# Performance work log

Measured on AMD Instinct MI355X. Metric: run time of the kernel, lower is better.

Reference implementation:

```python
import jax, jax.numpy as jnp
import numpy as np

D = 512       # d_model
H = 8         # n_heads
HD = D // H   # head_dim
LYR = 4       # number_of_layers
PMT = 20      # pmt_len
L = 2048      # decode / target length (src_len - pmt_len)
BS = 1
DOUT = 3      # d_output (3 coding classes)
DFF = 4 * D
EPS = 1e-5


def layer_norm(x, g, b):
    m = jnp.mean(x, axis=-1, keepdims=True)
    v = jnp.mean((x - m) ** 2, axis=-1, keepdims=True)
    return (x - m) * jax.lax.rsqrt(v + EPS) * g + b


def rope(x):
    # x: (b, h, s, hd); half-split rotary with base 10000, positions = arange(s)
    half = x.shape[-1] // 2
    pos = jnp.arange(x.shape[2], dtype=jnp.float32)
    inv_freq = 1.0 / (10000.0 ** (jnp.arange(half, dtype=jnp.float32) / half))
    ang = pos[:, None] * inv_freq[None, :]          # (s, half)
    cos = jnp.cos(ang)[None, None]                  # (1,1,s,half)
    sin = jnp.sin(ang)[None, None]
    x1, x2 = x[..., :half], x[..., half:]
    return jnp.concatenate([x1 * cos - x2 * sin, x1 * sin + x2 * cos], axis=-1)


def mha(xq, xkv, wqkv, bqkv, wo, bo, key_mask, causal):
    # xq: (b, sq, D), xkv: (b, sk, D); key_mask: (b, sk) with 1=valid
    b, sq, _ = xq.shape
    sk = xkv.shape[1]
    q = xq @ wqkv[:, :D] + bqkv[:D]
    kv = xkv @ wqkv[:, D:] + bqkv[D:]
    k, v = kv[..., :D], kv[..., D:]
    q = q.reshape(b, sq, H, HD).transpose(0, 2, 1, 3)   # (b,h,sq,hd)
    k = k.reshape(b, sk, H, HD).transpose(0, 2, 1, 3)
    v = v.reshape(b, sk, H, HD).transpose(0, 2, 1, 3)
    q = rope(q)
    k = rope(k)
    scores = jnp.einsum('bhqd,bhkd->bhqk', q, k) / jnp.sqrt(jnp.float32(HD))
    scores = scores + jnp.where(key_mask[:, None, None, :] > 0, 0.0, -1e9)
    if causal:
        cm = jnp.tril(jnp.ones((sq, sk), dtype=bool))
        scores = jnp.where(cm[None, None], scores, -1e9)
    attn = jax.nn.softmax(scores, axis=-1)
    out = jnp.einsum('bhqk,bhkd->bhqd', attn, v)
    out = out.transpose(0, 2, 1, 3).reshape(b, sq, D)
    return out @ wo + bo


def setup_inputs() -> dict:
    key = jax.random.key(0)
    ks = jax.random.split(key, 16)
    s = 0.02
    p = lambda i, shape: jax.random.normal(ks[i], shape, jnp.float32) * s
    return {
        'trg_inputs': jax.random.normal(ks[0], (BS, L, DOUT), jnp.float32),
        'src_rep': jax.random.normal(ks[1], (BS, PMT + L, D), jnp.float32),
        'src_mask': jnp.ones((BS, L), jnp.float32),
        'emb_w': p(2, (DOUT, D)), 'emb_b': jnp.zeros((D,), jnp.float32),
        'sa_wqkv': p(3, (LYR, D, 3 * D)), 'sa_bqkv': jnp.zeros((LYR, 3 * D), jnp.float32),
        'sa_wo': p(4, (LYR, D, D)), 'sa_bo': jnp.zeros((LYR, D), jnp.float32),
        'ca_wqkv': p(5, (LYR, D, 3 * D)), 'ca_bqkv': jnp.zeros((LYR, 3 * D), jnp.float32),
        'ca_wo': p(6, (LYR, D, D)), 'ca_bo': jnp.zeros((LYR, D), jnp.float32),
        'ffn_w1': p(7, (LYR, D, DFF)), 'ffn_b1': jnp.zeros((LYR, DFF), jnp.float32),
        'ffn_w2': p(8, (LYR, DFF, D)), 'ffn_b2': jnp.zeros((LYR, D), jnp.float32),
        'ln_g': jnp.ones((LYR, 3, D), jnp.float32), 'ln_b': jnp.zeros((LYR, 3, D), jnp.float32),
        'lnf_g': jnp.ones((D,), jnp.float32), 'lnf_b': jnp.zeros((D,), jnp.float32),
        'gen_w': p(9, (D, DOUT)), 'gen_b': jnp.zeros((DOUT,), jnp.float32),
    }


def reference(trg_inputs, src_rep, src_mask, emb_w, emb_b, sa_wqkv, sa_bqkv, sa_wo, sa_bo,
              ca_wqkv, ca_bqkv, ca_wo, ca_bo, ffn_w1, ffn_b1, ffn_w2, ffn_b2,
              ln_g, ln_b, lnf_g, lnf_b, gen_w, gen_b):
    srb = src_rep[:, PMT:, :]                       # (bs, L, D)
    x = trg_inputs @ emb_w + emb_b                  # (bs, L, D)
    trg_mask = src_mask                             # parallel mode: trg_mask = src_mask
    for li in range(LYR):
        h = layer_norm(x, ln_g[li, 0], ln_b[li, 0])
        x = x + mha(h, h, sa_wqkv[li], sa_bqkv[li], sa_wo[li], sa_bo[li], trg_mask, causal=True)
        h = layer_norm(x, ln_g[li, 1], ln_b[li, 1])
        x = x + mha(h, srb, ca_wqkv[li], ca_bqkv[li], ca_wo[li], ca_bo[li], src_mask, causal=False)
        h = layer_norm(x, ln_g[li, 2], ln_b[li, 2])
        x = x + (jax.nn.relu(h @ ffn_w1[li] + ffn_b1[li]) @ ffn_w2[li] + ffn_b2[li])
    x = layer_norm(x, lnf_g, lnf_b)
    return x @ gen_w + gen_b                        # logits (bs, L, 3)
```

## Files before the change

kernel.cpp:

```cpp
#include <hip/hip_runtime.h>
#include <hip/hip_bf16.h>

#define SEQ 2048
#define DM 512
#define NHEAD 8
#define HDIM 64
#define DFFN 2048
#define PMTN 20

typedef __bf16 bf16x8 __attribute__((ext_vector_type(8)));
typedef float f32x4 __attribute__((ext_vector_type(4)));
typedef unsigned short u16x8 __attribute__((ext_vector_type(8)));

__device__ __forceinline__ float wave_sum(float v) {
#pragma unroll
  for (int off = 32; off; off >>= 1) v += __shfl_xor(v, off);
  return v;
}

__device__ __forceinline__ unsigned short f2b(float x) {
  __hip_bfloat16 h = __float2bfloat16(x);
  return *(unsigned short*)&h;
}

__device__ __forceinline__ void gll16(const __hip_bfloat16* g, __hip_bfloat16* l) {
  __builtin_amdgcn_global_load_lds(
      (const __attribute__((address_space(1))) unsigned int*)(g),
      (__attribute__((address_space(3))) unsigned int*)(l), 16, 0, 0);
}

__global__ __launch_bounds__(256) void embed_kernel(
    const float* __restrict__ trg, const float* __restrict__ w,
    const float* __restrict__ b, float* __restrict__ X) {
  int idx = blockIdx.x * 256 + threadIdx.x;
  int r = idx >> 9, c = idx & 511;
  float t0 = trg[r * 3 + 0], t1 = trg[r * 3 + 1], t2 = trg[r * 3 + 2];
  X[idx] = t0 * w[c] + t1 * w[512 + c] + t2 * w[1024 + c] + b[c];
}

__global__ __launch_bounds__(256) void cast_bf16_kernel(
    const float* __restrict__ in, __hip_bfloat16* __restrict__ out) {
  int i = blockIdx.x * 256 + threadIdx.x;
  out[i] = __float2bfloat16(in[i]);
}

__global__ __launch_bounds__(256) void rope_table_kernel(float2* __restrict__ rt) {
  int idx = blockIdx.x * 256 + threadIdx.x;
  int row = idx >> 5, i = idx & 31;
  float inv = __expf(-(float)i * (9.210340371976184f / 32.f));
  float sn, cs;
  sincosf((float)row * inv, &sn, &cs);
  rt[idx] = make_float2(cs, sn);
}

__global__ __launch_bounds__(256) void mbias_kernel(
    const float* __restrict__ mask, float* __restrict__ mb) {
  int i = blockIdx.x * 256 + threadIdx.x;
  mb[i] = (mask[i] > 0.f) ? 0.f : -8.0e9f;
}

__global__ __launch_bounds__(256) void ln_bf16_kernel(
    const float* __restrict__ x, const float* __restrict__ g,
    const float* __restrict__ b, __hip_bfloat16* __restrict__ o) {
  int row = blockIdx.x * 4 + (threadIdx.x >> 6);
  int lane = threadIdx.x & 63;
  const float* xr = x + (long)row * DM;
  float v[8];
  float s = 0.f;
#pragma unroll
  for (int j = 0; j < 8; j++) { v[j] = xr[lane + 64 * j]; s += v[j]; }
  s = wave_sum(s);
  float mean = s * (1.f / DM);
  float q = 0.f;
#pragma unroll
  for (int j = 0; j < 8; j++) { float d = v[j] - mean; q += d * d; }
  q = wave_sum(q);
  float r = rsqrtf(q * (1.f / DM) + 1e-5f);
  __hip_bfloat16* orow = o + (long)row * DM;
#pragma unroll
  for (int j = 0; j < 8; j++) {
    int c = lane + 64 * j;
    orow[c] = __float2bfloat16((v[j] - mean) * r * g[c] + b[c]);
  }
}

__global__ __launch_bounds__(256) void ln_f32_kernel(
    const float* __restrict__ x, const float* __restrict__ g,
    const float* __restrict__ b, float* __restrict__ o) {
  int row = blockIdx.x * 4 + (threadIdx.x >> 6);
  int lane = threadIdx.x & 63;
  const float* xr = x + (long)row * DM;
  float v[8];
  float s = 0.f;
#pragma unroll
  for (int j = 0; j < 8; j++) { v[j] = xr[lane + 64 * j]; s += v[j]; }
  s = wave_sum(s);
  float mean = s * (1.f / DM);
  float q = 0.f;
#pragma unroll
  for (int j = 0; j < 8; j++) { float d = v[j] - mean; q += d * d; }
  q = wave_sum(q);
  float r = rsqrtf(q * (1.f / DM) + 1e-5f);
  float* orow = o + (long)row * DM;
#pragma unroll
  for (int j = 0; j < 8; j++) {
    int c = lane + 64 * j;
    orow[c] = (v[j] - mean) * r * g[c] + b[c];
  }
}

__global__ __launch_bounds__(256) void transpose_layer_kernel(
    const float* __restrict__ wqkv, const float* __restrict__ wo,
    const float* __restrict__ cwqkv, const float* __restrict__ cwo,
    const float* __restrict__ w1, const float* __restrict__ w2,
    __hip_bfloat16* __restrict__ Wt) {
  int b = blockIdx.x;
  const float* W;
  __hip_bfloat16* O;
  int Kd, Nd;
  if (b < 192)      { W = wqkv;  O = Wt + 0;       Kd = 512;  Nd = 1536; }
  else if (b < 256) { W = wo;    O = Wt + 786432;  Kd = 512;  Nd = 512;  b -= 192; }
  else if (b < 448) { W = cwqkv; O = Wt + 1048576; Kd = 512;  Nd = 1536; b -= 256; }
  else if (b < 512) { W = cwo;   O = Wt + 1835008; Kd = 512;  Nd = 512;  b -= 448; }
  else if (b < 768) { W = w1;    O = Wt + 2097152; Kd = 512;  Nd = 2048; b -= 512; }
  else              { W = w2;    O = Wt + 3145728; Kd = 2048; Nd = 512;  b -= 768; }
  int tn = Nd >> 6;
  int k0 = (b / tn) * 64, n0 = (b % tn) * 64;
  __shared__ float T[64][65];
  int t = threadIdx.x;
  int rr = t >> 4, c4 = (t & 15) * 4;
#pragma unroll
  for (int p = 0; p < 4; p++) {
    int row = rr + p * 16;
    float4 v = *(const float4*)(W + (long)(k0 + row) * Nd + n0 + c4);
    T[row][c4 + 0] = v.x; T[row][c4 + 1] = v.y;
    T[row][c4 + 2] = v.z; T[row][c4 + 3] = v.w;
  }
  __syncthreads();
#pragma unroll
  for (int p = 0; p < 4; p++) {
    int row = rr + p * 16;
    ushort4 pk;
    pk.x = f2b(T[c4 + 0][row]); pk.y = f2b(T[c4 + 1][row]);
    pk.z = f2b(T[c4 + 2][row]); pk.w = f2b(T[c4 + 3][row]);
    *(ushort4*)(O + (long)(n0 + row) * Kd + k0 + c4) = pk;
  }
}

__global__ __launch_bounds__(256) void gemm_bf16_64(
    const __hip_bfloat16* __restrict__ A, int lda,
    const __hip_bfloat16* __restrict__ Bt, int ldb,
    const float* __restrict__ bias,
    const float* __restrict__ residual,
    float* __restrict__ Cf, __hip_bfloat16* __restrict__ Cb,
    int ldc, int K, int relu) {
  __shared__ __attribute__((aligned(16))) __hip_bfloat16 As[2][4096];
  __shared__ __attribute__((aligned(16))) __hip_bfloat16 Bs[2][4096];
  const int t = threadIdx.x;
  const int n0 = blockIdx.x * 64, m0 = blockIdx.y * 64;
  const int w = t >> 6, lane = t & 63;
  const int wr = w >> 1, wc = w & 1;
  const int fr = lane & 15, fk = lane >> 4;
  const int r0 = t & 63, c0 = t >> 6;
  const __hip_bfloat16* Arow = A + (long)(m0 + r0) * lda;
  const __hip_bfloat16* Brow = Bt + (long)(n0 + r0) * ldb;

  uint4 ra0 = *(const uint4*)(Arow + c0 * 8);
  uint4 ra1 = *(const uint4*)(Arow + (c0 + 4) * 8);
  uint4 rb0 = *(const uint4*)(Brow + c0 * 8);
  uint4 rb1 = *(const uint4*)(Brow + (c0 + 4) * 8);
  *(uint4*)(&As[0][(c0 * 64 + r0) * 8]) = ra0;
  *(uint4*)(&As[0][((c0 + 4) * 64 + r0) * 8]) = ra1;
  *(uint4*)(&Bs[0][(c0 * 64 + r0) * 8]) = rb0;
  *(uint4*)(&Bs[0][((c0 + 4) * 64 + r0) * 8]) = rb1;
  __syncthreads();

  f32x4 acc[2][2] = {};
  const int NK = K >> 6;
  for (int ks = 0; ks < NK; ++ks) {
    const int cur = ks & 1;
    if (ks + 1 < NK) {
      const int ko = (ks + 1) << 6;
      ra0 = *(const uint4*)(Arow + ko + c0 * 8);
      ra1 = *(const uint4*)(Arow + ko + (c0 + 4) * 8);
      rb0 = *(const uint4*)(Brow + ko + c0 * 8);
      rb1 = *(const uint4*)(Brow + ko + (c0 + 4) * 8);
    }
#pragma unroll
    for (int kk = 0; kk < 2; ++kk) {
      const int kc = kk * 4 + fk;
      bf16x8 a0 = *(const bf16x8*)(&As[cur][(kc * 64 + wr * 32 + fr) * 8]);
      bf16x8 a1 = *(const bf16x8*)(&As[cur][(kc * 64 + wr * 32 + 16 + fr) * 8]);
      bf16x8 b0 = *(const bf16x8*)(&Bs[cur][(kc * 64 + wc * 32 + fr) * 8]);
      bf16x8 b1 = *(const bf16x8*)(&Bs[cur][(kc * 64 + wc * 32 + 16 + fr) * 8]);
      acc[0][0] = __builtin_amdgcn_mfma_f32_16x16x32_bf16(a0, b0, acc[0][0], 0, 0, 0);
      acc[0][1] = __builtin_amdgcn_mfma_f32_16x16x32_bf16(a0, b1, acc[0][1], 0, 0, 0);
      acc[1][0] = __builtin_amdgcn_mfma_f32_16x16x32_bf16(a1, b0, acc[1][0], 0, 0, 0);
      acc[1][1] = __builtin_amdgcn_mfma_f32_16x16x32_bf16(a1, b1, acc[1][1], 0, 0, 0);
    }
    if (ks + 1 < NK) {
      const int nxt = cur ^ 1;
      *(uint4*)(&As[nxt][(c0 * 64 + r0) * 8]) = ra0;
      *(uint4*)(&As[nxt][((c0 + 4) * 64 + r0) * 8]) = ra1;
      *(uint4*)(&Bs[nxt][(c0 * 64 + r0) * 8]) = rb0;
      *(uint4*)(&Bs[nxt][((c0 + 4) * 64 + r0) * 8]) = rb1;
    }
    __syncthreads();
  }

#pragma unroll
  for (int m = 0; m < 2; ++m)
#pragma unroll
    for (int n = 0; n < 2; ++n)
#pragma unroll
      for (int j = 0; j < 4; ++j) {
        int r = m0 + wr * 32 + m * 16 + fk * 4 + j;
        int c = n0 + wc * 32 + n * 16 + fr;
        float v = acc[m][n][j] + bias[c];
        if (relu) v = fmaxf(v, 0.f);
        if (residual) v += residual[(long)r * ldc + c];
        if (Cf) Cf[(long)r * ldc + c] = v;
        if (Cb) Cb[(long)r * ldc + c] = __float2bfloat16(v);
      }
}

__global__ __launch_bounds__(256) void pack_kernel(
    const __hip_bfloat16* __restrict__ qsrc, int ldq,
    const __hip_bfloat16* __restrict__ ksrc, int ldk,
    const __hip_bfloat16* __restrict__ vsrc, int ldv,
    const float2* __restrict__ rt,
    __hip_bfloat16* __restrict__ Qp, __hip_bfloat16* __restrict__ Kp,
    __hip_bfloat16* __restrict__ Vp) {
  const int row = blockIdx.x;
  const int t = threadIdx.x;
  const int h = t >> 5, i = t & 31;
  float2 cs = rt[row * 32 + i];
  const long dsto = ((long)h * SEQ + row) * 64 + i;
  {
    const __hip_bfloat16* p = qsrc + (long)row * ldq + h * 64;
    float a = __bfloat162float(p[i]), b = __bfloat162float(p[i + 32]);
    Qp[dsto] = __float2bfloat16(a * cs.x - b * cs.y);
    Qp[dsto + 32] = __float2bfloat16(a * cs.y + b * cs.x);
  }
  {
    const __hip_bfloat16* p = ksrc + (long)row * ldk + h * 64;
    float a = __bfloat162float(p[i]), b = __bfloat162float(p[i + 32]);
    Kp[dsto] = __float2bfloat16(a * cs.x - b * cs.y);
    Kp[dsto + 32] = __float2bfloat16(a * cs.y + b * cs.x);
  }
  {
    const __hip_bfloat16* p = vsrc + (long)row * ldv + h * 64;
    Vp[dsto] = p[i];
    Vp[dsto + 32] = p[i + 32];
  }
}

__global__ __launch_bounds__(256) void attn_part_kernel(
    const __hip_bfloat16* __restrict__ Qp, const __hip_bfloat16* __restrict__ Kp,
    const __hip_bfloat16* __restrict__ Vp, const float* __restrict__ mbias,
    __hip_bfloat16* __restrict__ Op, float* __restrict__ Ml,
    int causal, int csz) {
  const int qt = blockIdx.x, ch = blockIdx.y, head = blockIdx.z;
  const int kv0 = ch * csz;
  if (causal && kv0 > qt * 64 + 63) return;
  const int kvlen = causal ? min(csz, qt * 64 + 64 - kv0) : csz;
  const int nt = (kvlen + 63) >> 6;

  __shared__ __attribute__((aligned(16))) __hip_bfloat16 Ks[4096];
  __shared__ __attribute__((aligned(16))) __hip_bfloat16 Vt[4096];
  __shared__ __attribute__((aligned(16))) __hip_bfloat16 Ps[4096];
  const int t = threadIdx.x, w = t >> 6, lane = t & 63;
  const int fr = lane & 15, fk = lane >> 4;
  const int qr = qt * 64 + w * 16 + fr;
  const int wq0 = qt * 64 + w * 16;
  const float SCL = 0.18033688011112042f;

  bf16x8 qa0, qa1;
  {
    const __hip_bfloat16* qp = Qp + ((long)head * SEQ + qr) * 64 + fk * 8;
    qa0 = *(const bf16x8*)qp;
    qa1 = *(const bf16x8*)(qp + 32);
  }
  const __hip_bfloat16* Kh = Kp + (long)head * SEQ * 64;
  const __hip_bfloat16* Vh = Vp + (long)head * SEQ * 64;

  float m_i = -3e38f, l_i = 0.f;
  f32x4 o_[4] = {};
  const int sw2 = (fr & 7) << 4;

  const int skrow = t & 63, skc = t >> 6;
  const int vr = t & 31, vc = (t >> 5) & 7;

  for (int tile = 0; tile < nt; ++tile) {
    const int kb = kv0 + tile * 64;
    __syncthreads();
    {
      const __hip_bfloat16* src = Kh + (long)(kb + skrow) * 64 + skc * 8;
      gll16(src, Ks + t * 8);
      gll16(src + 32, Ks + t * 8 + 2048);
    }
    {
      const __hip_bfloat16* vp = Vh + (long)(kb + 2 * vr) * 64 + vc * 8;
      u16x8 v0 = *(const u16x8*)vp;
      u16x8 v1 = *(const u16x8*)(vp + 64);
#pragma unroll
      for (int e = 0; e < 8; e++) {
        int d = vc * 8 + e;
        ushort2 hh;
        hh.x = v0[e]; hh.y = v1[e];
        *(ushort2*)((char*)Vt + ((d * 128 + 4 * vr) ^ (e << 4))) = hh;
      }
    }
    __syncthreads();

    const bool need = !causal || (kb <= wq0 + 15);
    if (need) {
      const bool diag = causal && (kb + 63 > wq0);

      f32x4 sacc[4];
#pragma unroll
      for (int n = 0; n < 4; n++) {
        bf16x8 ka0 = *(const bf16x8*)(Ks + fk * 512 + (n * 16 + fr) * 8);
        bf16x8 ka1 = *(const bf16x8*)(Ks + (4 + fk) * 512 + (n * 16 + fr) * 8);
        f32x4 zz = {};
        zz = __builtin_amdgcn_mfma_f32_16x16x32_bf16(ka0, qa0, zz, 0, 0, 0);
        sacc[n] = __builtin_amdgcn_mfma_f32_16x16x32_bf16(ka1, qa1, zz, 0, 0, 0);
      }

      float sv[4][4];
      float rm = -3e38f;
#pragma unroll
      for (int n = 0; n < 4; n++) {
        const int ka = kb + n * 16 + fk * 4;
        float4 mb = *(const float4*)(mbias + ka);
        sv[n][0] = sacc[n][0] + mb.x;
        sv[n][1] = sacc[n][1] + mb.y;
        sv[n][2] = sacc[n][2] + mb.z;
        sv[n][3] = sacc[n][3] + mb.w;
        if (diag) {
#pragma unroll
          for (int j = 0; j < 4; j++)
            if (ka + j > qr) sv[n][j] = -3e38f;
        }
#pragma unroll
        for (int j = 0; j < 4; j++) rm = fmaxf(rm, sv[n][j]);
      }
      rm = fmaxf(rm, __shfl_xor(rm, 16));
      rm = fmaxf(rm, __shfl_xor(rm, 32));
      if (!__all(rm <= m_i)) {
        float nm = fmaxf(m_i, rm);
        float f = exp2f((m_i - nm) * SCL);
        l_i *= f;
#pragma unroll
        for (int n = 0; n < 4; n++) o_[n] *= f;
        m_i = nm;
      }
      float ps = 0.f;
#pragma unroll
      for (int n = 0; n < 4; n++) {
        float p0 = exp2f((sv[n][0] - m_i) * SCL);
        float p1 = exp2f((sv[n][1] - m_i) * SCL);
        float p2 = exp2f((sv[n][2] - m_i) * SCL);
        float p3 = exp2f((sv[n][3] - m_i) * SCL);
        ps += (p0 + p1) + (p2 + p3);
        ushort4 pk4;
        pk4.x = f2b(p0); pk4.y = f2b(p1); pk4.z = f2b(p2); pk4.w = f2b(p3);
        *(ushort4*)((char*)Ps + ((w * 2048 + fr * 128 + (n * 16 + fk * 4) * 2) ^ sw2)) = pk4;
      }
      ps += __shfl_xor(ps, 16);
      ps += __shfl_xor(ps, 32);
      l_i += ps;

#pragma unroll
      for (int s = 0; s < 2; s++) {
        bf16x8 pb = *(const bf16x8*)((char*)Ps + ((w * 2048 + fr * 128 + s * 64 + fk * 16) ^ sw2));
#pragma unroll
        for (int n = 0; n < 4; n++) {
          bf16x8 va = *(const bf16x8*)((char*)Vt + (((n * 16 + fr) * 128 + s * 64 + fk * 16) ^ sw2));
          o_[n] = __builtin_amdgcn_mfma_f32_16x16x32_bf16(va, pb, o_[n], 0, 0, 0);
        }
      }
    }
  }

  const long bid = ((long)head * 32 + qt) * gridDim.y + ch;
  __hip_bfloat16* Ob = Op + bid * 4096;
#pragma unroll
  for (int n = 0; n < 4; n++) {
    ushort4 ov;
    ov.x = f2b(o_[n][0]); ov.y = f2b(o_[n][1]);
    ov.z = f2b(o_[n][2]); ov.w = f2b(o_[n][3]);
    *(ushort4*)(Ob + (w * 16 + fr) * 64 + n * 16 + fk * 4) = ov;
  }
  if (fk == 0) {
    float2 ml = make_float2(m_i, l_i);
    *(float2*)(Ml + bid * 128 + (w * 16 + fr) * 2) = ml;
  }
}

__global__ __launch_bounds__(256) void attn_combine_kernel(
    const __hip_bfloat16* __restrict__ Op, const float* __restrict__ Ml,
    __hip_bfloat16* __restrict__ O, int ldo, int causal, int csz, int nch) {
  const int qt = blockIdx.x, head = blockIdx.y;
  const int nc = causal ? min(nch, (qt * 64 + 63) / csz + 1) : nch;
  const int t = threadIdx.x;
  const int row = t >> 2, c16 = (t & 3) * 16;
  const long bid0 = ((long)head * 32 + qt) * nch;
  const float SCL = 0.18033688011112042f;
  float M = -3e38f;
  for (int c = 0; c < nc; c++) M = fmaxf(M, Ml[(bid0 + c) * 128 + row * 2]);
  float L = 0.f;
  float acc[16] = {};
  for (int c = 0; c < nc; c++) {
    float2 ml = *(const float2*)(Ml + (bid0 + c) * 128 + row * 2);
    float wg = exp2f((ml.x - M) * SCL);
    L += wg * ml.y;
    const __hip_bfloat16* base = Op + (bid0 + c) * 4096 + row * 64 + c16;
    bf16x8 a = *(const bf16x8*)base;
    bf16x8 b = *(const bf16x8*)(base + 8);
#pragma unroll
    for (int e = 0; e < 8; e++) {
      acc[e] += wg * (float)a[e];
      acc[8 + e] += wg * (float)b[e];
    }
  }
  float invL = 1.f / fmaxf(L, 1e-20f);
  u16x8 o0, o1;
#pragma unroll
  for (int e = 0; e < 8; e++) {
    o0[e] = f2b(acc[e] * invL);
    o1[e] = f2b(acc[8 + e] * invL);
  }
  __hip_bfloat16* orow = O + (long)(qt * 64 + row) * ldo + head * 64 + c16;
  *(u16x8*)orow = o0;
  *(u16x8*)(orow + 8) = o1;
}

__global__ __launch_bounds__(64) void gen_kernel(
    const float* __restrict__ h, const float* __restrict__ gw,
    const float* __restrict__ gb, float* __restrict__ out) {
  int row = blockIdx.x, lane = threadIdx.x;
  float a0 = 0.f, a1 = 0.f, a2 = 0.f;
  for (int k = lane; k < DM; k += 64) {
    float x = h[(long)row * DM + k];
    a0 = fmaf(x, gw[k * 3 + 0], a0);
    a1 = fmaf(x, gw[k * 3 + 1], a1);
    a2 = fmaf(x, gw[k * 3 + 2], a2);
  }
  a0 = wave_sum(a0);
  a1 = wave_sum(a1);
  a2 = wave_sum(a2);
  if (lane == 0) {
    out[row * 3 + 0] = a0 + gb[0];
    out[row * 3 + 1] = a1 + gb[1];
    out[row * 3 + 2] = a2 + gb[2];
  }
}

extern "C" void kernel_launch(void* const* d_in, const int* in_sizes, int n_in,
                              void* d_out, int out_size, void* d_ws, size_t ws_size,
                              hipStream_t stream) {
  const float* trg      = (const float*)d_in[0];
  const float* src_rep  = (const float*)d_in[1];
  const float* src_mask = (const float*)d_in[2];
  const float* emb_w    = (const float*)d_in[3];
  const float* emb_b    = (const float*)d_in[4];
  const float* sa_wqkv  = (const float*)d_in[5];
  const float* sa_bqkv  = (const float*)d_in[6];
  const float* sa_wo    = (const float*)d_in[7];
  const float* sa_bo    = (const float*)d_in[8];
  const float* ca_wqkv  = (const float*)d_in[9];
  const float* ca_bqkv  = (const float*)d_in[10];
  const float* ca_wo    = (const float*)d_in[11];
  const float* ca_bo    = (const float*)d_in[12];
  const float* ffn_w1   = (const float*)d_in[13];
  const float* ffn_b1   = (const float*)d_in[14];
  const float* ffn_w2   = (const float*)d_in[15];
  const float* ffn_b2   = (const float*)d_in[16];
  const float* ln_g     = (const float*)d_in[17];
  const float* ln_b     = (const float*)d_in[18];
  const float* lnf_g    = (const float*)d_in[19];
  const float* lnf_b    = (const float*)d_in[20];
  const float* gen_w    = (const float*)d_in[21];
  const float* gen_b    = (const float*)d_in[22];

  const float* srb = src_rep + (long)PMTN * DM;

  char* wsb = (char*)d_ws;
  float*          X    = (float*)wsb;
  __hip_bfloat16* Hb   = (__hip_bfloat16*)(wsb + (4ul << 20));
  __hip_bfloat16* QKV  = (__hip_bfloat16*)(wsb + (6ul << 20));
  __hip_bfloat16* AO   = (__hip_bfloat16*)(wsb + (12ul << 20));
  __hip_bfloat16* SRBb = (__hip_bfloat16*)(wsb + (14ul << 20));
  __hip_bfloat16* Wt   = (__hip_bfloat16*)(wsb + (16ul << 20));
  float2*         rt   = (float2*)(wsb + (24ul << 20));
  float*          mbias= (float*)(wsb + (24ul << 20) + 524288);
  __hip_bfloat16* Qp   = (__hip_bfloat16*)(wsb + (25ul << 20));
  __hip_bfloat16* Kp   = (__hip_bfloat16*)(wsb + (27ul << 20));
  __hip_bfloat16* Vp   = (__hip_bfloat16*)(wsb + (29ul << 20));
  __hip_bfloat16* Op   = (__hip_bfloat16*)(wsb + (31ul << 20));
  float*          Ml   = (float*)(wsb + (39ul << 20));
  __hip_bfloat16* MID  = QKV;
  float*          Hf   = (float*)QKV;

  const int nch = 4;
  const int csz = SEQ / nch;

  embed_kernel<<<(SEQ * DM) / 256, 256, 0, stream>>>(trg, emb_w, emb_b, X);
  cast_bf16_kernel<<<(SEQ * DM) / 256, 256, 0, stream>>>(srb, SRBb);
  rope_table_kernel<<<256, 256, 0, stream>>>(rt);
  mbias_kernel<<<8, 256, 0, stream>>>(src_mask, mbias);

  __hip_bfloat16* wqkvT  = Wt + 0;
  __hip_bfloat16* woT    = Wt + 786432;
  __hip_bfloat16* cwqkvT = Wt + 1048576;
  __hip_bfloat16* cwoT   = Wt + 1835008;
  __hip_bfloat16* w1T    = Wt + 2097152;
  __hip_bfloat16* w2T    = Wt + 3145728;

  for (int li = 0; li < 4; li++) {
    transpose_layer_kernel<<<1024, 256, 0, stream>>>(
        sa_wqkv + (long)li * DM * 3 * DM, sa_wo + (long)li * DM * DM,
        ca_wqkv + (long)li * DM * 3 * DM, ca_wo + (long)li * DM * DM,
        ffn_w1 + (long)li * DM * DFFN, ffn_w2 + (long)li * DFFN * DM, Wt);

    const float* bqkv  = sa_bqkv + (long)li * 3 * DM;
    const float* bo    = sa_bo + (long)li * DM;
    const float* cbqkv = ca_bqkv + (long)li * 3 * DM;
    const float* cbo   = ca_bo + (long)li * DM;
    const float* b1    = ffn_b1 + (long)li * DFFN;
    const float* b2    = ffn_b2 + (long)li * DM;
    const float* g0  = ln_g + (long)(li * 3 + 0) * DM;
    const float* bb0 = ln_b + (long)(li * 3 + 0) * DM;
    const float* g1  = ln_g + (long)(li * 3 + 1) * DM;
    const float* bb1 = ln_b + (long)(li * 3 + 1) * DM;
    const float* g2  = ln_g + (long)(li * 3 + 2) * DM;
    const float* bb2 = ln_b + (long)(li * 3 + 2) * DM;

    ln_bf16_kernel<<<512, 256, 0, stream>>>(X, g0, bb0, Hb);
    gemm_bf16_64<<<dim3(24, 32), 256, 0, stream>>>(
        Hb, DM, wqkvT, DM, bqkv, nullptr, nullptr, QKV, 3 * DM, DM, 0);
    pack_kernel<<<SEQ, 256, 0, stream>>>(
        QKV, 3 * DM, QKV + DM, 3 * DM, QKV + 2 * DM, 3 * DM, rt, Qp, Kp, Vp);
    attn_part_kernel<<<dim3(32, nch, 8), 256, 0, stream>>>(
        Qp, Kp, Vp, mbias, Op, Ml, 1, csz);
    attn_combine_kernel<<<dim3(32, 8), 256, 0, stream>>>(
        Op, Ml, AO, DM, 1, csz, nch);
    gemm_bf16_64<<<dim3(8, 32), 256, 0, stream>>>(
        AO, DM, woT, DM, bo, X, X, nullptr, DM, DM, 0);

    ln_bf16_kernel<<<512, 256, 0, stream>>>(X, g1, bb1, Hb);
    __hip_bfloat16* Qc  = QKV;
    __hip_bfloat16* KVc = QKV + (long)SEQ * DM;
    gemm_bf16_64<<<dim3(8, 32), 256, 0, stream>>>(
        Hb, DM, cwqkvT, DM, cbqkv, nullptr, nullptr, Qc, DM, DM, 0);
    gemm_bf16_64<<<dim3(16, 32), 256, 0, stream>>>(
        SRBb, DM, cwqkvT + (long)DM * DM, DM, cbqkv + DM, nullptr, nullptr,
        KVc, 2 * DM, DM, 0);
    pack_kernel<<<SEQ, 256, 0, stream>>>(
        Qc, DM, KVc, 2 * DM, KVc + DM, 2 * DM, rt, Qp, Kp, Vp);
    attn_part_kernel<<<dim3(32, nch, 8), 256, 0, stream>>>(
        Qp, Kp, Vp, mbias, Op, Ml, 0, csz);
    attn_combine_kernel<<<dim3(32, 8), 256, 0, stream>>>(
        Op, Ml, AO, DM, 0, csz, nch);
    gemm_bf16_64<<<dim3(8, 32), 256, 0, stream>>>(
        AO, DM, cwoT, DM, cbo, X, X, nullptr, DM, DM, 0);

    ln_bf16_kernel<<<512, 256, 0, stream>>>(X, g2, bb2, Hb);
    gemm_bf16_64<<<dim3(32, 32), 256, 0, stream>>>(
        Hb, DM, w1T, DM, b1, nullptr, nullptr, MID, DFFN, DM, 1);
    gemm_bf16_64<<<dim3(8, 32), 256, 0, stream>>>(
        MID, DFFN, w2T, DFFN, b2, X, X, nullptr, DM, DFFN, 0);
  }

  ln_f32_kernel<<<512, 256, 0, stream>>>(X, lnf_g, lnf_b, Hf);
  gen_kernel<<<SEQ, 64, 0, stream>>>(Hf, gen_w, gen_b, (float*)d_out);
}
```

Baseline: 872.3 us.

## Fuse RoPE and head packing into QKV GEMM epilogue with pre-transposed V

The QKV projection GEMM now stages its output tile in shared memory and writes Q and K directly in per-head layout with rotary embedding applied. V is written pre-transposed (head, dim, seq), which removes the separate pack kernel and the intermediate QKV buffer round trip. The cross-attention Q and KV projections are merged into one launch by selecting the A operand per block column. Attention loads the pre-transposed V with async global-to-LDS copies instead of transposing it in registers. The GEMM epilogue gains extra LDS traffic and branching, and the workspace layout is reshuffled.

```diff
diff --git a/kernel.cpp b/kernel.cpp
--- a/kernel.cpp
+++ b/kernel.cpp
@@ -149,21 +149,29 @@
 
 __global__ __launch_bounds__(256) void gemm_bf16_64(
     const __hip_bfloat16* __restrict__ A, int lda,
+    const __hip_bfloat16* __restrict__ A2,
     const __hip_bfloat16* __restrict__ Bt, int ldb,
     const float* __restrict__ bias,
     const float* __restrict__ residual,
-    float* __restrict__ Cf, __hip_bfloat16* __restrict__ Cb,
-    int ldc, int K, int relu) {
+    float* __restrict__ Cf, __hip_bfloat16* __restrict__ Cb, int ldc,
+    int K, int relu, int mode, const float2* __restrict__ rt,
+    __hip_bfloat16* __restrict__ Qp, __hip_bfloat16* __restrict__ Kp,
+    __hip_bfloat16* __restrict__ Vtp) {
   __shared__ __attribute__((aligned(16))) __hip_bfloat16 As[2][4096];
   __shared__ __attribute__((aligned(16))) __hip_bfloat16 Bs[2][4096];
   const int t = threadIdx.x;
-  const int n0 = blockIdx.x * 64, m0 = blockIdx.y * 64;
+  const int bx = blockIdx.x;
+  const int nrow = bx * 64, m0 = blockIdx.y * 64;
+  const int ptype = (mode == 0) ? 3 : (nrow < 512 ? 0 : (nrow < 1024 ? 1 : 2));
+  const int head = (nrow >> 6) & 7;
+  const __hip_bfloat16* Ause = (mode == 2 && bx >= 8) ? A2 : A;
+
   const int w = t >> 6, lane = t & 63;
   const int wr = w >> 1, wc = w & 1;
   const int fr = lane & 15, fk = lane >> 4;
   const int r0 = t & 63, c0 = t >> 6;
-  const __hip_bfloat16* Arow = A + (long)(m0 + r0) * lda;
-  const __hip_bfloat16* Brow = Bt + (long)(n0 + r0) * ldb;
+  const __hip_bfloat16* Arow = Ause + (long)(m0 + r0) * lda;
+  const __hip_bfloat16* Brow = Bt + (long)(nrow + r0) * ldb;
 
   uint4 ra0 = *(const uint4*)(Arow + c0 * 8);
   uint4 ra1 = *(const uint4*)(Arow + (c0 + 4) * 8);
@@ -208,56 +216,70 @@
     __syncthreads();
   }
 
+  if (ptype == 3) {
+#pragma unroll
+    for (int m = 0; m < 2; ++m)
+#pragma unroll
+      for (int n = 0; n < 2; ++n)
+#pragma unroll
+        for (int j = 0; j < 4; ++j) {
+          int r = m0 + wr * 32 + m * 16 + fk * 4 + j;
+          int c = nrow + wc * 32 + n * 16 + fr;
+          float v = acc[m][n][j] + bias[c];
+          if (relu) v = fmaxf(v, 0.f);
+          if (residual) v += residual[(long)r * ldc + c];
+          if (Cf) Cf[(long)r * ldc + c] = v;
+          if (Cb) Cb[(long)r * ldc + c] = __float2bfloat16(v);
+        }
+    return;
+  }
+
+  float* Lt = (float*)As;
 #pragma unroll
   for (int m = 0; m < 2; ++m)
 #pragma unroll
     for (int n = 0; n < 2; ++n)
 #pragma unroll
       for (int j = 0; j < 4; ++j) {
-        int r = m0 + wr * 32 + m * 16 + fk * 4 + j;
-        int c = n0 + wc * 32 + n * 16 + fr;
-        float v = acc[m][n][j] + bias[c];
-        if (relu) v = fmaxf(v, 0.f);
-        if (residual) v += residual[(long)r * ldc + c];
-        if (Cf) Cf[(long)r * ldc + c] = v;
-        if (Cb) Cb[(long)r * ldc + c] = __float2bfloat16(v);
+        int rl = wr * 32 + m * 16 + fk * 4 + j;
+        int cl = wc * 32 + n * 16 + fr;
+        Lt[rl * 64 + (cl ^ (rl & 31))] = acc[m][n][j] + bias[nrow + cl];
       }
-}
-
-__global__ __launch_bounds__(256) void pack_kernel(
-    const __hip_bfloat16* __restrict__ qsrc, int ldq,
-    const __hip_bfloat16* __restrict__ ksrc, int ldk,
-    const __hip_bfloat16* __restrict__ vsrc, int ldv,
-    const float2* __restrict__ rt,
-    __hip_bfloat16* __restrict__ Qp, __hip_bfloat16* __restrict__ Kp,
-    __hip_bfloat16* __restrict__ Vp) {
-  const int row = blockIdx.x;
-  const int t = threadIdx.x;
-  const int h = t >> 5, i = t & 31;
-  float2 cs = rt[row * 32 + i];
-  const long dsto = ((long)h * SEQ + row) * 64 + i;
-  {
-    const __hip_bfloat16* p = qsrc + (long)row * ldq + h * 64;
-    float a = __bfloat162float(p[i]), b = __bfloat162float(p[i + 32]);
-    Qp[dsto] = __float2bfloat16(a * cs.x - b * cs.y);
-    Qp[dsto + 32] = __float2bfloat16(a * cs.y + b * cs.x);
-  }
-  {
-    const __hip_bfloat16* p = ksrc + (long)row * ldk + h * 64;
-    float a = __bfloat162float(p[i]), b = __bfloat162float(p[i + 32]);
-    Kp[dsto] = __float2bfloat16(a * cs.x - b * cs.y);
-    Kp[dsto + 32] = __float2bfloat16(a * cs.y + b * cs.x);
-  }
-  {
-    const __hip_bfloat16* p = vsrc + (long)row * ldv + h * 64;
-    Vp[dsto] = p[i];
-    Vp[dsto + 32] = p[i + 32];
+  __syncthreads();
+
+  if (ptype == 2) {
+    const int d = t >> 2, sc = (t & 3) * 16;
+    u16x8 o0, o1;
+#pragma unroll
+    for (int s = 0; s < 8; s++) {
+      o0[s] = f2b(Lt[(sc + s) * 64 + (d ^ ((sc + s) & 31))]);
+      o1[s] = f2b(Lt[(sc + 8 + s) * 64 + (d ^ ((sc + 8 + s) & 31))]);
+    }
+    __hip_bfloat16* dst = Vtp + ((long)(head * 64 + d)) * SEQ + m0 + sc;
+    *(u16x8*)dst = o0;
+    *(u16x8*)(dst + 8) = o1;
+  } else {
+    const int r = t >> 2, i0 = (t & 3) * 8;
+    const float2* rp = rt + (long)(m0 + r) * 32 + i0;
+    u16x8 lo, hi;
+#pragma unroll
+    for (int p = 0; p < 8; p++) {
+      float a = Lt[r * 64 + ((i0 + p) ^ (r & 31))];
+      float b = Lt[r * 64 + ((i0 + p + 32) ^ (r & 31))];
+      float2 cs = rp[p];
+      lo[p] = f2b(a * cs.x - b * cs.y);
+      hi[p] = f2b(a * cs.y + b * cs.x);
+    }
+    __hip_bfloat16* dst =
+        (ptype == 0 ? Qp : Kp) + ((long)head * SEQ + m0 + r) * 64 + i0;
+    *(u16x8*)dst = lo;
+    *(u16x8*)(dst + 32) = hi;
   }
 }
 
 __global__ __launch_bounds__(256) void attn_part_kernel(
     const __hip_bfloat16* __restrict__ Qp, const __hip_bfloat16* __restrict__ Kp,
-    const __hip_bfloat16* __restrict__ Vp, const float* __restrict__ mbias,
+    const __hip_bfloat16* __restrict__ Vtp, const float* __restrict__ mbias,
     __hip_bfloat16* __restrict__ Op, float* __restrict__ Ml,
     int causal, int csz) {
   const int qt = blockIdx.x, ch = blockIdx.y, head = blockIdx.z;
@@ -267,7 +289,7 @@
   const int nt = (kvlen + 63) >> 6;
 
   __shared__ __attribute__((aligned(16))) __hip_bfloat16 Ks[4096];
-  __shared__ __attribute__((aligned(16))) __hip_bfloat16 Vt[4096];
+  __shared__ __attribute__((aligned(16))) __hip_bfloat16 Vs[4096];
   __shared__ __attribute__((aligned(16))) __hip_bfloat16 Ps[4096];
   const int t = threadIdx.x, w = t >> 6, lane = t & 63;
   const int fr = lane & 15, fk = lane >> 4;
@@ -282,34 +304,24 @@
     qa1 = *(const bf16x8*)(qp + 32);
   }
   const __hip_bfloat16* Kh = Kp + (long)head * SEQ * 64;
-  const __hip_bfloat16* Vh = Vp + (long)head * SEQ * 64;
+  const __hip_bfloat16* Vh = Vtp + (long)head * 64 * SEQ;
 
   float m_i = -3e38f, l_i = 0.f;
   f32x4 o_[4] = {};
   const int sw2 = (fr & 7) << 4;
-
-  const int skrow = t & 63, skc = t >> 6;
-  const int vr = t & 31, vc = (t >> 5) & 7;
 
   for (int tile = 0; tile < nt; ++tile) {
     const int kb = kv0 + tile * 64;
     __syncthreads();
     {
-      const __hip_bfloat16* src = Kh + (long)(kb + skrow) * 64 + skc * 8;
+      const __hip_bfloat16* src = Kh + (long)(kb + (t & 63)) * 64 + (t >> 6) * 8;
       gll16(src, Ks + t * 8);
       gll16(src + 32, Ks + t * 8 + 2048);
     }
     {
-      const __hip_bfloat16* vp = Vh + (long)(kb + 2 * vr) * 64 + vc * 8;
-      u16x8 v0 = *(const u16x8*)vp;
-      u16x8 v1 = *(const u16x8*)(vp + 64);
-#pragma unroll
-      for (int e = 0; e < 8; e++) {
-        int d = vc * 8 + e;
-        ushort2 hh;
-        hh.x = v0[e]; hh.y = v1[e];
-        *(ushort2*)((char*)Vt + ((d * 128 + 4 * vr) ^ (e << 4))) = hh;
-      }
+      const __hip_bfloat16* src = Vh + (long)(t & 63) * SEQ + kb + (t >> 6) * 8;
+      gll16(src, Vs + t * 8);
+      gll16(src + 32, Vs + t * 8 + 2048);
     }
     __syncthreads();
 
@@ -376,7 +388,7 @@
         bf16x8 pb = *(const bf16x8*)((char*)Ps + ((w * 2048 + fr * 128 + s * 64 + fk * 16) ^ sw2));
 #pragma unroll
         for (int n = 0; n < 4; n++) {
-          bf16x8 va = *(const bf16x8*)((char*)Vt + (((n * 16 + fr) * 128 + s * 64 + fk * 16) ^ sw2));
+          bf16x8 va = *(const bf16x8*)(Vs + (s * 4 + fk) * 512 + (n * 16 + fr) * 8);
           o_[n] = __builtin_amdgcn_mfma_f32_16x16x32_bf16(va, pb, o_[n], 0, 0, 0);
         }
       }
@@ -489,19 +501,18 @@
   char* wsb = (char*)d_ws;
   float*          X    = (float*)wsb;
   __hip_bfloat16* Hb   = (__hip_bfloat16*)(wsb + (4ul << 20));
-  __hip_bfloat16* QKV  = (__hip_bfloat16*)(wsb + (6ul << 20));
-  __hip_bfloat16* AO   = (__hip_bfloat16*)(wsb + (12ul << 20));
-  __hip_bfloat16* SRBb = (__hip_bfloat16*)(wsb + (14ul << 20));
-  __hip_bfloat16* Wt   = (__hip_bfloat16*)(wsb + (16ul << 20));
-  float2*         rt   = (float2*)(wsb + (24ul << 20));
-  float*          mbias= (float*)(wsb + (24ul << 20) + 524288);
-  __hip_bfloat16* Qp   = (__hip_bfloat16*)(wsb + (25ul << 20));
-  __hip_bfloat16* Kp   = (__hip_bfloat16*)(wsb + (27ul << 20));
-  __hip_bfloat16* Vp   = (__hip_bfloat16*)(wsb + (29ul << 20));
-  __hip_bfloat16* Op   = (__hip_bfloat16*)(wsb + (31ul << 20));
-  float*          Ml   = (float*)(wsb + (39ul << 20));
-  __hip_bfloat16* MID  = QKV;
-  float*          Hf   = (float*)QKV;
+  __hip_bfloat16* MID  = (__hip_bfloat16*)(wsb + (6ul << 20));
+  __hip_bfloat16* Op   = MID;
+  float*          Hf   = (float*)MID;
+  __hip_bfloat16* AO   = (__hip_bfloat16*)(wsb + (14ul << 20));
+  __hip_bfloat16* SRBb = (__hip_bfloat16*)(wsb + (16ul << 20));
+  __hip_bfloat16* Wt   = (__hip_bfloat16*)(wsb + (18ul << 20));
+  float2*         rt   = (float2*)(wsb + (26ul << 20));
+  float*          mbias= (float*)(wsb + (26ul << 20) + 524288);
+  float*          Ml   = (float*)(wsb + (27ul << 20));
+  __hip_bfloat16* Qp   = (__hip_bfloat16*)(wsb + (28ul << 20));
+  __hip_bfloat16* Kp   = (__hip_bfloat16*)(wsb + (30ul << 20));
+  __hip_bfloat16* Vtp  = (__hip_bfloat16*)(wsb + (32ul << 20));
 
   const int nch = 4;
   const int csz = SEQ / nch;
@@ -539,38 +550,35 @@
 
     ln_bf16_kernel<<<512, 256, 0, stream>>>(X, g0, bb0, Hb);
     gemm_bf16_64<<<dim3(24, 32), 256, 0, stream>>>(
-        Hb, DM, wqkvT, DM, bqkv, nullptr, nullptr, QKV, 3 * DM, DM, 0);
-    pack_kernel<<<SEQ, 256, 0, stream>>>(
-        QKV, 3 * DM, QKV + DM, 3 * DM, QKV + 2 * DM, 3 * DM, rt, Qp, Kp, Vp);
+        Hb, DM, nullptr, wqkvT, DM, bqkv, nullptr, nullptr, nullptr, DM,
+        DM, 0, 1, rt, Qp, Kp, Vtp);
     attn_part_kernel<<<dim3(32, nch, 8), 256, 0, stream>>>(
-        Qp, Kp, Vp, mbias, Op, Ml, 1, csz);
+        Qp, Kp, Vtp, mbias, Op, Ml, 1, csz);
     attn_combine_kernel<<<dim3(32, 8), 256, 0, stream>>>(
         Op, Ml, AO, DM, 1, csz, nch);
     gemm_bf16_64<<<dim3(8, 32), 256, 0, stream>>>(
-        AO, DM, woT, DM, bo, X, X, nullptr, DM, DM, 0);
+        AO, DM, nullptr, woT, DM, bo, X, X, nullptr, DM,
+        DM, 0, 0, nullptr, nullptr, nullptr, nullptr);
 
     ln_bf16_kernel<<<512, 256, 0, stream>>>(X, g1, bb1, Hb);
-    __hip_bfloat16* Qc  = QKV;
-    __hip_bfloat16* KVc = QKV + (long)SEQ * DM;
-    gemm_bf16_64<<<dim3(8, 32), 256, 0, stream>>>(
-        Hb, DM, cwqkvT, DM, cbqkv, nullptr, nullptr, Qc, DM, DM, 0);
-    gemm_bf16_64<<<dim3(16, 32), 256, 0, stream>>>(
-        SRBb, DM, cwqkvT + (long)DM * DM, DM, cbqkv + DM, nullptr, nullptr,
-        KVc, 2 * DM, DM, 0);
-    pack_kernel<<<SEQ, 256, 0, stream>>>(
-        Qc, DM, KVc, 2 * DM, KVc + DM, 2 * DM, rt, Qp, Kp, Vp);
+    gemm_bf16_64<<<dim3(24, 32), 256, 0, stream>>>(
+        Hb, DM, SRBb, cwqkvT, DM, cbqkv, nullptr, nullptr, nullptr, DM,
+        DM, 0, 2, rt, Qp, Kp, Vtp);
     attn_part_kernel<<<dim3(32, nch, 8), 256, 0, stream>>>(
-        Qp, Kp, Vp, mbias, Op, Ml, 0, csz);
+        Qp, Kp, Vtp, mbias, Op, Ml, 0, csz);
     attn_combine_kernel<<<dim3(32, 8), 256, 0, stream>>>(
         Op, Ml, AO, DM, 0, csz, nch);
     gemm_bf16_64<<<dim3(8, 32), 256, 0, stream>>>(
-        AO, DM, cwoT, DM, cbo, X, X, nullptr, DM, DM, 0);
+        AO, DM, nullptr, cwoT, DM, cbo, X, X, nullptr, DM,
+        DM, 0, 0, nullptr, nullptr, nullptr, nullptr);
 
     ln_bf16_kernel<<<512, 256, 0, stream>>>(X, g2, bb2, Hb);
     gemm_bf16_64<<<dim3(32, 32), 256, 0, stream>>>(
-        Hb, DM, w1T, DM, b1, nullptr, nullptr, MID, DFFN, DM, 1);
+        Hb, DM, nullptr, w1T, DM, b1, nullptr, nullptr, MID, DFFN,
+        DM, 1, 0, nullptr, nullptr, nullptr, nullptr);
     gemm_bf16_64<<<dim3(8, 32), 256, 0, stream>>>(
-        MID, DFFN, w2T, DFFN, b2, X, X, nullptr, DM, DFFN, 0);
+        MID, DFFN, nullptr, w2T, DFFN, b2, X, X, nullptr, DM,
+        DFFN, 0, 0, nullptr, nullptr, nullptr, nullptr);
   }
 
   ln_f32_kernel<<<512, 256, 0, stream>>>(X, lnf_g, lnf_b, Hf);
```

Result: faster. 802.5 us (-8.0%).
